# Kernel optimization log

Measured on AMD Instinct MI355X. Metric: run time of the kernel, lower is better.

## Reference

```python
import jax, jax.numpy as jnp
import numpy as np
from jax.ops import segment_sum

NUM_NODES = 100000
HIDDEN = 128
NUM_LAYERS = 3
EDGES = 640000
BN_EPS = 1e-5


def setup_inputs() -> dict:
    key = jax.random.key(0)
    ks = jax.random.split(key, 6)
    edge_index = jax.random.randint(ks[0], (2, EDGES), 0, NUM_NODES, dtype=jnp.int32)
    # xavier-ish init for embedding (hidden-1 dims; last dim is log-degree feature)
    emb_weight = jax.random.normal(ks[1], (NUM_NODES, HIDDEN - 1), dtype=jnp.float32) * 0.02
    # GCNConv linear weights [L, in, out] and biases [L, out]
    Ws = jax.random.normal(ks[2], (NUM_LAYERS, HIDDEN, HIDDEN), dtype=jnp.float32) * (1.0 / np.sqrt(HIDDEN))
    bs = jnp.zeros((NUM_LAYERS, HIDDEN), dtype=jnp.float32)
    gammas = jnp.ones((NUM_LAYERS, HIDDEN), dtype=jnp.float32)
    betas = jnp.zeros((NUM_LAYERS, HIDDEN), dtype=jnp.float32)
    return {"emb_weight": emb_weight, "Ws": Ws, "bs": bs,
            "gammas": gammas, "betas": betas, "edge_index": edge_index}


def reference(emb_weight, Ws, bs, gammas, betas, edge_index):
    row, col = edge_index[0], edge_index[1]  # source, target
    N = emb_weight.shape[0]
    ones_e = jnp.ones(row.shape[0], dtype=emb_weight.dtype)

    # node_degree_features = log(out_degree + 1) (degree of edge_index[0])
    deg_src = segment_sum(ones_e, row, num_segments=N)
    x = jnp.concatenate([emb_weight, jnp.log(deg_src + 1.0)[:, None]], axis=1)  # [N, H]

    # GCN symmetric normalization (add_self_loops=False): deg over targets
    deg = segment_sum(ones_e, col, num_segments=N)
    dinv = jnp.where(deg > 0, jax.lax.rsqrt(jnp.maximum(deg, 1.0)), 0.0)
    norm = dinv[row] * dinv[col]  # [E]

    for i in range(Ws.shape[0]):
        x_prev = x
        h = x @ Ws[i]  # [N, H]
        # scatter-add of normalized messages: out[col] += norm * h[row]
        agg = segment_sum(norm[:, None] * h[row], col, num_segments=N) + bs[i]
        # BatchNorm1d (batch statistics, biased variance)
        mean = agg.mean(axis=0)
        var = agg.var(axis=0)
        x = gammas[i] * (agg - mean) * jax.lax.rsqrt(var + BN_EPS) + betas[i]
        x = jax.nn.relu(x)
        if i > 0:
            x = x + 0.5 * x_prev
    return x
```

## Files before the change

kernel.cpp:

```cpp
#include <hip/hip_runtime.h>
#include <hip/hip_bf16.h>
#include <math.h>

#define BN_EPS 1e-5f

typedef __attribute__((ext_vector_type(8))) short short8v;
typedef __attribute__((ext_vector_type(4))) float f32x4;

__device__ inline float bf_lo(unsigned int p) { return __uint_as_float(p << 16); }
__device__ inline float bf_hi(unsigned int p) { return __uint_as_float(p & 0xffff0000u); }
__device__ inline unsigned int packbf(float a, float b) {
    unsigned short lo = __builtin_bit_cast(unsigned short, __float2bfloat16(a));
    unsigned short hi = __builtin_bit_cast(unsigned short, __float2bfloat16(b));
    return (unsigned int)lo | ((unsigned int)hi << 16);
}


__global__ __launch_bounds__(256) void deg_kernel(const int* __restrict__ row, const int* __restrict__ col,
                                                  float* __restrict__ deg_src, float* __restrict__ deg_dst, int E) {
    int e = blockIdx.x * 256 + threadIdx.x;
    if (e < E) {
        atomicAdd(&deg_src[row[e]], 1.0f);
        atomicAdd(&deg_dst[col[e]], 1.0f);
    }
}

__global__ __launch_bounds__(256) void dinv_cnt_kernel(float* __restrict__ deg_dst, int* __restrict__ cnt, int N) {
    int n = blockIdx.x * 256 + threadIdx.x;
    if (n < N) {
        float d = deg_dst[n];
        cnt[n] = (int)d;
        deg_dst[n] = (d > 0.0f) ? rsqrtf(d) : 0.0f;
    }
}

__global__ __launch_bounds__(256) void initx_kernel(const float* __restrict__ emb, const float* __restrict__ deg_src,
                                                    unsigned int* __restrict__ x, int N) {
    int idx = blockIdx.x * 256 + threadIdx.x;
    if (idx < N * 64) {
        int n = idx >> 6, p = idx & 63;
        float v0, v1;
        if (p < 63) {
            v0 = emb[(size_t)n * 127 + 2 * p];
            v1 = emb[(size_t)n * 127 + 2 * p + 1];
        } else {
            v0 = emb[(size_t)n * 127 + 126];
            v1 = logf(deg_src[n] + 1.0f);
        }
        x[idx] = packbf(v0, v1);
    }
}

__global__ __launch_bounds__(256) void wt_kernel(const float* __restrict__ Ws, __hip_bfloat16* __restrict__ Wt) {
    int idx = blockIdx.x * 256 + threadIdx.x;
    if (idx < 3 * 16384) {
        int l = idx >> 14, rem = idx & 16383, c = rem >> 7, k = rem & 127;
        Wt[idx] = __float2bfloat16(Ws[(l << 14) + (k << 7) + c]);
    }
}


__global__ __launch_bounds__(256) void scan_pass1(const int* __restrict__ cnt, int* __restrict__ blockSums,
                                                  int N, int PT) {
    __shared__ int lds[256];
    const int tid = threadIdx.x;
    const int start = (blockIdx.x * 256 + tid) * PT;
    int s = 0;
    for (int i = 0; i < PT; ++i) {
        int idx = start + i;
        if (idx < N) s += cnt[idx];
    }
    lds[tid] = s;
    __syncthreads();
    for (int d = 128; d > 0; d >>= 1) {
        if (tid < d) lds[tid] += lds[tid + d];
        __syncthreads();
    }
    if (tid == 0) blockSums[blockIdx.x] = lds[0];
}

__global__ __launch_bounds__(256) void scan_pass2(const int* __restrict__ blockSums, int* __restrict__ blockOffs) {
    __shared__ int lds[256];
    const int tid = threadIdx.x;
    int v = blockSums[tid];
    lds[tid] = v;
    __syncthreads();
    for (int d = 1; d < 256; d <<= 1) {
        int t = (tid >= d) ? lds[tid - d] : 0;
        __syncthreads();
        lds[tid] += t;
        __syncthreads();
    }
    blockOffs[tid] = lds[tid] - v;
}

__global__ __launch_bounds__(256) void scan_pass3(const int* __restrict__ cnt, const int* __restrict__ blockOffs,
                                                  int* __restrict__ off, int* __restrict__ cur,
                                                  int N, int PT, int E) {
    __shared__ int lds[256];
    const int tid = threadIdx.x;
    const int start = (blockIdx.x * 256 + tid) * PT;
    int s = 0;
    for (int i = 0; i < PT; ++i) {
        int idx = start + i;
        if (idx < N) s += cnt[idx];
    }
    lds[tid] = s;
    __syncthreads();
    for (int d = 1; d < 256; d <<= 1) {
        int t = (tid >= d) ? lds[tid - d] : 0;
        __syncthreads();
        lds[tid] += t;
        __syncthreads();
    }
    int prefix = blockOffs[blockIdx.x] + lds[tid] - s;
    for (int i = 0; i < PT; ++i) {
        int idx = start + i;
        if (idx < N) {
            off[idx] = prefix;
            cur[idx] = prefix;
            prefix += cnt[idx];
        }
    }
    if (blockIdx.x == 0 && tid == 0) off[N] = E;
}

__global__ __launch_bounds__(256) void fill_kernel(const int* __restrict__ row, const int* __restrict__ col,
                                                   const float* __restrict__ dinv, int* __restrict__ cur,
                                                   int2* __restrict__ meta, int E) {
    int e = blockIdx.x * 256 + threadIdx.x;
    if (e < E) {
        int r = row[e], t = col[e];
        int p = atomicAdd(&cur[t], 1);
        meta[p] = make_int2(r, __float_as_int(dinv[r] * dinv[t]));
    }
}


__global__ __launch_bounds__(256) void gemm_mfma(const __hip_bfloat16* __restrict__ X,
                                                 const __hip_bfloat16* __restrict__ Wt,
                                                 __hip_bfloat16* __restrict__ H, float* __restrict__ sums,
                                                 int nStripes, int N) {
    if (blockIdx.x == 0) sums[threadIdx.x] = 0.0f;

    const int lane = threadIdx.x & 63;
    const int wv = threadIdx.x >> 6;
    const int r = lane & 15;
    const int q = lane >> 4;
    const int ch = (blockIdx.x * 4 + wv) & 1;

    short8v bfrag[4][4];
#pragma unroll
    for (int ct = 0; ct < 4; ++ct)
#pragma unroll
        for (int kk = 0; kk < 4; ++kk)
            bfrag[ct][kk] = *(const short8v*)(Wt + ((ch * 64 + ct * 16 + r) << 7) + kk * 32 + q * 8);

    const int totalJobs = nStripes * 2;
    for (int job = blockIdx.x * 4 + wv; job < totalJobs; job += gridDim.x * 4) {
        const int s = job >> 1;
        const int arow = s * 16 + r;
        short8v a0 = {}, a1 = {}, a2 = {}, a3 = {};
        if (arow < N) {
            const __hip_bfloat16* xp = X + ((size_t)arow << 7) + q * 8;
            a0 = *(const short8v*)(xp);
            a1 = *(const short8v*)(xp + 32);
            a2 = *(const short8v*)(xp + 64);
            a3 = *(const short8v*)(xp + 96);
        }
        f32x4 acc[4];
#pragma unroll
        for (int ct = 0; ct < 4; ++ct) {
            f32x4 c = {0.f, 0.f, 0.f, 0.f};
            c = __builtin_amdgcn_mfma_f32_16x16x32_bf16(a0, bfrag[ct][0], c, 0, 0, 0);
            c = __builtin_amdgcn_mfma_f32_16x16x32_bf16(a1, bfrag[ct][1], c, 0, 0, 0);
            c = __builtin_amdgcn_mfma_f32_16x16x32_bf16(a2, bfrag[ct][2], c, 0, 0, 0);
            c = __builtin_amdgcn_mfma_f32_16x16x32_bf16(a3, bfrag[ct][3], c, 0, 0, 0);
            acc[ct] = c;
        }
#pragma unroll
        for (int g = 0; g < 4; ++g) {
            int grow = s * 16 + q * 4 + g;
            if (grow < N) {
                __hip_bfloat16* hp = H + ((size_t)grow << 7) + ch * 64 + r;
#pragma unroll
                for (int ct = 0; ct < 4; ++ct)
                    hp[ct * 16] = __float2bfloat16(acc[ct][g]);
            }
        }
    }
}


__global__ __launch_bounds__(256) void gather_kernel(const __hip_bfloat16* __restrict__ h,
                                                     const int* __restrict__ off, const int2* __restrict__ meta,
                                                     const float* __restrict__ bias,
                                                     unsigned int* __restrict__ aggb, float* __restrict__ sums, int N) {
    __shared__ float sm[2][4][128];
    const int tid = threadIdx.x;
    const int lane = tid & 63;
    const int w = tid >> 6;
    const int g = lane >> 4;
    const int s = lane & 15;

    float b8[8];
    *(float4*)&b8[0] = *(const float4*)&bias[s * 8];
    *(float4*)&b8[4] = *(const float4*)&bias[s * 8 + 4];

    float psum[8], psq[8];
#pragma unroll
    for (int j = 0; j < 8; ++j) { psum[j] = 0.f; psq[j] = 0.f; }

    for (int base = (blockIdx.x * 4 + w) * 2; base < N; base += gridDim.x * 8) {
        const int nA = __builtin_amdgcn_readfirstlane(base);
        const int hasB = (nA + 1 < N);
        const int sA = off[nA];
        const int eA = off[nA + 1];
        const int eB = hasB ? off[nA + 2] : eA;

        float accA[8], accB[8];
#pragma unroll
        for (int j = 0; j < 8; ++j) { accA[j] = 0.f; accB[j] = 0.f; }

        int iA = sA, iB = eA;
        while (iA < eA || iB < eB) {
            int i0A = iA + g, i1A = iA + 4 + g;
            int i0B = iB + g, i1B = iB + 4 + g;
            int idx0A = (i0A < eA) ? i0A : 0;
            int idx1A = (i1A < eA) ? i1A : 0;
            int idx0B = (i0B < eB) ? i0B : 0;
            int idx1B = (i1B < eB) ? i1B : 0;
            int2 m0A = meta[idx0A], m1A = meta[idx1A];
            int2 m0B = meta[idx0B], m1B = meta[idx1B];
            float w0A = (i0A < eA) ? __int_as_float(m0A.y) : 0.f;
            float w1A = (i1A < eA) ? __int_as_float(m1A.y) : 0.f;
            float w0B = (i0B < eB) ? __int_as_float(m0B.y) : 0.f;
            float w1B = (i1B < eB) ? __int_as_float(m1B.y) : 0.f;
            short8v h0A = *(const short8v*)(h + ((size_t)m0A.x << 7) + s * 8);
            short8v h1A = *(const short8v*)(h + ((size_t)m1A.x << 7) + s * 8);
            short8v h0B = *(const short8v*)(h + ((size_t)m0B.x << 7) + s * 8);
            short8v h1B = *(const short8v*)(h + ((size_t)m1B.x << 7) + s * 8);
#pragma unroll
            for (int j = 0; j < 4; ++j) {
                unsigned int u;
                u = ((const unsigned int*)&h0A)[j];
                accA[2 * j]     = fmaf(w0A, bf_lo(u), accA[2 * j]);
                accA[2 * j + 1] = fmaf(w0A, bf_hi(u), accA[2 * j + 1]);
                u = ((const unsigned int*)&h1A)[j];
                accA[2 * j]     = fmaf(w1A, bf_lo(u), accA[2 * j]);
                accA[2 * j + 1] = fmaf(w1A, bf_hi(u), accA[2 * j + 1]);
                u = ((const unsigned int*)&h0B)[j];
                accB[2 * j]     = fmaf(w0B, bf_lo(u), accB[2 * j]);
                accB[2 * j + 1] = fmaf(w0B, bf_hi(u), accB[2 * j + 1]);
                u = ((const unsigned int*)&h1B)[j];
                accB[2 * j]     = fmaf(w1B, bf_lo(u), accB[2 * j]);
                accB[2 * j + 1] = fmaf(w1B, bf_hi(u), accB[2 * j + 1]);
            }
            iA += 8; iB += 8;
        }
#pragma unroll
        for (int j = 0; j < 8; ++j) {
            accA[j] += __shfl_xor(accA[j], 16);
            accA[j] += __shfl_xor(accA[j], 32);
            accA[j] += b8[j];
            accB[j] += __shfl_xor(accB[j], 16);
            accB[j] += __shfl_xor(accB[j], 32);
            accB[j] += b8[j];
        }
        if (g == 0) {
            unsigned int pk[4];
#pragma unroll
            for (int j = 0; j < 4; ++j) pk[j] = packbf(accA[2 * j], accA[2 * j + 1]);
            *(uint4*)(aggb + ((size_t)nA << 6) + s * 4) = *(uint4*)pk;
#pragma unroll
            for (int j = 0; j < 8; ++j) {
                psum[j] += accA[j];
                psq[j] = fmaf(accA[j], accA[j], psq[j]);
            }
            if (hasB) {
#pragma unroll
                for (int j = 0; j < 8; ++j) {
                    psum[j] += accB[j];
                    psq[j] = fmaf(accB[j], accB[j], psq[j]);
                }
            }
        } else if (g == 1 && hasB) {
            unsigned int pk[4];
#pragma unroll
            for (int j = 0; j < 4; ++j) pk[j] = packbf(accB[2 * j], accB[2 * j + 1]);
            *(uint4*)(aggb + ((size_t)(nA + 1) << 6) + s * 4) = *(uint4*)pk;
        }
    }
    if (g == 0) {
#pragma unroll
        for (int j = 0; j < 8; ++j) {
            sm[0][w][s * 8 + j] = psum[j];
            sm[1][w][s * 8 + j] = psq[j];
        }
    }
    __syncthreads();
    if (tid < 128) {
        atomicAdd(&sums[tid], sm[0][0][tid] + sm[0][1][tid] + sm[0][2][tid] + sm[0][3][tid]);
    } else {
        int c = tid - 128;
        atomicAdd(&sums[128 + c], sm[1][0][c] + sm[1][1][c] + sm[1][2][c] + sm[1][3][c]);
    }
}


template <int MODE>
__global__ __launch_bounds__(256) void bn_apply(const uint4* __restrict__ aggb, const float* __restrict__ sums,
                                                const float* __restrict__ gamma, const float* __restrict__ beta,
                                                const uint4* __restrict__ xprev, void* __restrict__ xout,
                                                int NO, float invN) {
    int idx = blockIdx.x * 256 + threadIdx.x;
    if (idx >= NO) return;
    const int c0 = (idx & 15) * 8;

    float su[8], sq[8], gm[8], bt[8];
    *(float4*)&su[0] = *(const float4*)&sums[c0];
    *(float4*)&su[4] = *(const float4*)&sums[c0 + 4];
    *(float4*)&sq[0] = *(const float4*)&sums[128 + c0];
    *(float4*)&sq[4] = *(const float4*)&sums[128 + c0 + 4];
    *(float4*)&gm[0] = *(const float4*)&gamma[c0];
    *(float4*)&gm[4] = *(const float4*)&gamma[c0 + 4];
    *(float4*)&bt[0] = *(const float4*)&beta[c0];
    *(float4*)&bt[4] = *(const float4*)&beta[c0 + 4];

    float sc[8], sh[8];
#pragma unroll
    for (int j = 0; j < 8; ++j) {
        float m = su[j] * invN;
        float v = sq[j] * invN - m * m;
        float inv = rsqrtf(fmaxf(v, 0.0f) + BN_EPS);
        sc[j] = gm[j] * inv;
        sh[j] = bt[j] - m * sc[j];
    }

    uint4 av = aggb[idx];
    const unsigned int* au = (const unsigned int*)&av;
    float r[8];
#pragma unroll
    for (int j = 0; j < 4; ++j) {
        r[2 * j]     = fmaxf(fmaf(bf_lo(au[j]), sc[2 * j],     sh[2 * j]),     0.f);
        r[2 * j + 1] = fmaxf(fmaf(bf_hi(au[j]), sc[2 * j + 1], sh[2 * j + 1]), 0.f);
    }
    if (MODE >= 1) {
        uint4 xv = xprev[idx];
        const unsigned int* xu = (const unsigned int*)&xv;
#pragma unroll
        for (int j = 0; j < 4; ++j) {
            r[2 * j]     = fmaf(0.5f, bf_lo(xu[j]), r[2 * j]);
            r[2 * j + 1] = fmaf(0.5f, bf_hi(xu[j]), r[2 * j + 1]);
        }
    }
    if (MODE == 2) {
        float* op = (float*)xout + (size_t)idx * 8;
        *(float4*)op       = make_float4(r[0], r[1], r[2], r[3]);
        *(float4*)(op + 4) = make_float4(r[4], r[5], r[6], r[7]);
    } else {
        unsigned int pk[4];
#pragma unroll
        for (int j = 0; j < 4; ++j) pk[j] = packbf(r[2 * j], r[2 * j + 1]);
        ((uint4*)xout)[idx] = *(uint4*)pk;
    }
}


extern "C" void kernel_launch(void* const* d_in, const int* in_sizes, int n_in,
                              void* d_out, int out_size, void* d_ws, size_t ws_size,
                              hipStream_t stream) {
    const float* emb    = (const float*)d_in[0];
    const float* Ws     = (const float*)d_in[1];
    const float* bs     = (const float*)d_in[2];
    const float* gammas = (const float*)d_in[3];
    const float* betas  = (const float*)d_in[4];
    const int*   ei     = (const int*)d_in[5];

    const int N = in_sizes[0] / 127;
    const int E = in_sizes[5] / 2;
    const int* row = ei;
    const int* col = ei + E;
    float* out = (float*)d_out;

    const size_t NH = (size_t)N * 128;
    __hip_bfloat16* XA = (__hip_bfloat16*)d_ws;
    __hip_bfloat16* XB = XA + NH;
    unsigned int*  AGG = (unsigned int*)(XB + NH);
    int2*         meta = (int2*)(AGG + NH / 2);
    __hip_bfloat16* Wt = (__hip_bfloat16*)(meta + E);
    float* deg_src = (float*)(Wt + 3 * 16384);
    float* dinvb   = deg_src + N;
    float* sums    = dinvb + N;
    int*   cnt     = (int*)(sums + 256);
    int*   cur     = cnt + N;
    int*   blockSums = cur + N;
    int*   blockOffs = blockSums + 256;
    int*   off     = blockOffs + 256;

    const int NO = (int)(NH / 8);
    const int PT = (N + 65535) / 65536;
    const int nStripes = (N + 15) / 16;
    const float invN = 1.0f / (float)N;

    hipMemsetAsync(deg_src, 0, sizeof(float) * 2 * (size_t)N, stream);
    wt_kernel<<<(3 * 16384 + 255) / 256, 256, 0, stream>>>(Ws, Wt);
    deg_kernel<<<(E + 255) / 256, 256, 0, stream>>>(row, col, deg_src, dinvb, E);
    dinv_cnt_kernel<<<(N + 255) / 256, 256, 0, stream>>>(dinvb, cnt, N);
    initx_kernel<<<(N * 64 + 255) / 256, 256, 0, stream>>>(emb, deg_src, (unsigned int*)XA, N);
    scan_pass1<<<256, 256, 0, stream>>>(cnt, blockSums, N, PT);
    scan_pass2<<<1, 256, 0, stream>>>(blockSums, blockOffs);
    scan_pass3<<<256, 256, 0, stream>>>(cnt, blockOffs, off, cur, N, PT, E);
    fill_kernel<<<(E + 255) / 256, 256, 0, stream>>>(row, col, dinvb, cur, meta, E);

    const __hip_bfloat16* xin[3]  = {XA, XA, XB};
    __hip_bfloat16*       hbuf[3] = {XB, XB, XA};

    for (int i = 0; i < 3; ++i) {
        gemm_mfma<<<1024, 256, 0, stream>>>(xin[i], Wt + (size_t)i * 16384, hbuf[i], sums, nStripes, N);
        gather_kernel<<<2048, 256, 0, stream>>>(hbuf[i], off, meta, bs + i * 128, AGG, sums, N);
        if (i == 0)
            bn_apply<0><<<(NO + 255) / 256, 256, 0, stream>>>((const uint4*)AGG, sums, gammas, betas,
                                                              (const uint4*)xin[i], (void*)XA, NO, invN);
        else if (i == 1)
            bn_apply<1><<<(NO + 255) / 256, 256, 0, stream>>>((const uint4*)AGG, sums, gammas + 128, betas + 128,
                                                              (const uint4*)xin[i], (void*)XB, NO, invN);
        else
            bn_apply<2><<<(NO + 255) / 256, 256, 0, stream>>>((const uint4*)AGG, sums, gammas + 256, betas + 256,
                                                              (const uint4*)xin[i], (void*)out, NO, invN);
    }
}
```

Before: 445.7 us.

## Map one node per 16-lane group in gather and fold dinv into fill

The gather kernel now gives each 16-lane quarter-wave its own destination node (4 nodes per wave), instead of splitting each node's edges across the four lane groups and combining them with shuffles. Each group issues up to 8 independent meta and row loads up front for more memory-level parallelism, then runs a serial tail loop for higher-degree nodes. The separate dinv/count kernel is dropped: the scan reads float degrees directly and fill computes the rsqrt inline. The workspace is also reordered so the int4 offset loads are aligned. The per-node serial tail adds divergence inside a wave when node degrees differ.

```diff
diff --git a/kernel.cpp b/kernel.cpp
--- a/kernel.cpp
+++ b/kernel.cpp
@@ -22,15 +22,6 @@
     if (e < E) {
         atomicAdd(&deg_src[row[e]], 1.0f);
         atomicAdd(&deg_dst[col[e]], 1.0f);
-    }
-}
-
-__global__ __launch_bounds__(256) void dinv_cnt_kernel(float* __restrict__ deg_dst, int* __restrict__ cnt, int N) {
-    int n = blockIdx.x * 256 + threadIdx.x;
-    if (n < N) {
-        float d = deg_dst[n];
-        cnt[n] = (int)d;
-        deg_dst[n] = (d > 0.0f) ? rsqrtf(d) : 0.0f;
     }
 }
 
@@ -60,7 +51,7 @@
 }
 
 
-__global__ __launch_bounds__(256) void scan_pass1(const int* __restrict__ cnt, int* __restrict__ blockSums,
+__global__ __launch_bounds__(256) void scan_pass1(const float* __restrict__ deg, int* __restrict__ blockSums,
                                                   int N, int PT) {
     __shared__ int lds[256];
     const int tid = threadIdx.x;
@@ -68,7 +59,7 @@
     int s = 0;
     for (int i = 0; i < PT; ++i) {
         int idx = start + i;
-        if (idx < N) s += cnt[idx];
+        if (idx < N) s += (int)deg[idx];
     }
     lds[tid] = s;
     __syncthreads();
@@ -94,7 +85,7 @@
     blockOffs[tid] = lds[tid] - v;
 }
 
-__global__ __launch_bounds__(256) void scan_pass3(const int* __restrict__ cnt, const int* __restrict__ blockOffs,
+__global__ __launch_bounds__(256) void scan_pass3(const float* __restrict__ deg, const int* __restrict__ blockOffs,
                                                   int* __restrict__ off, int* __restrict__ cur,
                                                   int N, int PT, int E) {
     __shared__ int lds[256];
@@ -103,7 +94,7 @@
     int s = 0;
     for (int i = 0; i < PT; ++i) {
         int idx = start + i;
-        if (idx < N) s += cnt[idx];
+        if (idx < N) s += (int)deg[idx];
     }
     lds[tid] = s;
     __syncthreads();
@@ -119,20 +110,23 @@
         if (idx < N) {
             off[idx] = prefix;
             cur[idx] = prefix;
-            prefix += cnt[idx];
+            prefix += (int)deg[idx];
         }
     }
     if (blockIdx.x == 0 && tid == 0) off[N] = E;
 }
 
 __global__ __launch_bounds__(256) void fill_kernel(const int* __restrict__ row, const int* __restrict__ col,
-                                                   const float* __restrict__ dinv, int* __restrict__ cur,
+                                                   const float* __restrict__ deg_dst, int* __restrict__ cur,
                                                    int2* __restrict__ meta, int E) {
     int e = blockIdx.x * 256 + threadIdx.x;
     if (e < E) {
         int r = row[e], t = col[e];
         int p = atomicAdd(&cur[t], 1);
-        meta[p] = make_int2(r, __float_as_int(dinv[r] * dinv[t]));
+        float dr = deg_dst[r], dt = deg_dst[t];
+        float ir = (dr > 0.0f) ? rsqrtf(dr) : 0.0f;
+        float it = (dt > 0.0f) ? rsqrtf(dt) : 0.0f;
+        meta[p] = make_int2(r, __float_as_int(ir * it));
     }
 }
 
@@ -211,85 +205,75 @@
 #pragma unroll
     for (int j = 0; j < 8; ++j) { psum[j] = 0.f; psq[j] = 0.f; }
 
-    for (int base = (blockIdx.x * 4 + w) * 2; base < N; base += gridDim.x * 8) {
+    for (int base = (blockIdx.x * 4 + w) * 4; base < N; base += gridDim.x * 16) {
         const int nA = __builtin_amdgcn_readfirstlane(base);
-        const int hasB = (nA + 1 < N);
-        const int sA = off[nA];
-        const int eA = off[nA + 1];
-        const int eB = hasB ? off[nA + 2] : eA;
-
-        float accA[8], accB[8];
-#pragma unroll
-        for (int j = 0; j < 8; ++j) { accA[j] = 0.f; accB[j] = 0.f; }
-
-        int iA = sA, iB = eA;
-        while (iA < eA || iB < eB) {
-            int i0A = iA + g, i1A = iA + 4 + g;
-            int i0B = iB + g, i1B = iB + 4 + g;
-            int idx0A = (i0A < eA) ? i0A : 0;
-            int idx1A = (i1A < eA) ? i1A : 0;
-            int idx0B = (i0B < eB) ? i0B : 0;
-            int idx1B = (i1B < eB) ? i1B : 0;
-            int2 m0A = meta[idx0A], m1A = meta[idx1A];
-            int2 m0B = meta[idx0B], m1B = meta[idx1B];
-            float w0A = (i0A < eA) ? __int_as_float(m0A.y) : 0.f;
-            float w1A = (i1A < eA) ? __int_as_float(m1A.y) : 0.f;
-            float w0B = (i0B < eB) ? __int_as_float(m0B.y) : 0.f;
-            float w1B = (i1B < eB) ? __int_as_float(m1B.y) : 0.f;
-            short8v h0A = *(const short8v*)(h + ((size_t)m0A.x << 7) + s * 8);
-            short8v h1A = *(const short8v*)(h + ((size_t)m1A.x << 7) + s * 8);
-            short8v h0B = *(const short8v*)(h + ((size_t)m0B.x << 7) + s * 8);
-            short8v h1B = *(const short8v*)(h + ((size_t)m1B.x << 7) + s * 8);
+        int4 o4 = *(const int4*)&off[nA];
+        int  o5 = off[nA + 4];
+        const bool nodeValid = (nA + g) < N;
+        int sG = (g < 2) ? ((g == 0) ? o4.x : o4.y) : ((g == 2) ? o4.z : o4.w);
+        int eG = (g < 2) ? ((g == 0) ? o4.y : o4.z) : ((g == 2) ? o4.w : o5);
+        if (!nodeValid) { sG = 0; eG = 0; }
+
+        int   rr[8];
+        float wgt[8];
+#pragma unroll
+        for (int t = 0; t < 8; ++t) {
+            int i = sG + t;
+            int idx = (i < eG) ? i : 0;
+            int2 m = meta[idx];
+            rr[t] = m.x;
+            wgt[t] = (i < eG) ? __int_as_float(m.y) : 0.0f;
+        }
+        uint4 hv[8];
+#pragma unroll
+        for (int t = 0; t < 8; ++t)
+            hv[t] = *(const uint4*)(h + ((size_t)rr[t] << 7) + s * 8);
+
+        float acc[8];
+#pragma unroll
+        for (int j = 0; j < 8; ++j) acc[j] = 0.f;
+#pragma unroll
+        for (int t = 0; t < 8; ++t) {
+            const unsigned int* u = (const unsigned int*)&hv[t];
 #pragma unroll
             for (int j = 0; j < 4; ++j) {
-                unsigned int u;
-                u = ((const unsigned int*)&h0A)[j];
-                accA[2 * j]     = fmaf(w0A, bf_lo(u), accA[2 * j]);
-                accA[2 * j + 1] = fmaf(w0A, bf_hi(u), accA[2 * j + 1]);
-                u = ((const unsigned int*)&h1A)[j];
-                accA[2 * j]     = fmaf(w1A, bf_lo(u), accA[2 * j]);
-                accA[2 * j + 1] = fmaf(w1A, bf_hi(u), accA[2 * j + 1]);
-                u = ((const unsigned int*)&h0B)[j];
-                accB[2 * j]     = fmaf(w0B, bf_lo(u), accB[2 * j]);
-                accB[2 * j + 1] = fmaf(w0B, bf_hi(u), accB[2 * j + 1]);
-                u = ((const unsigned int*)&h1B)[j];
-                accB[2 * j]     = fmaf(w1B, bf_lo(u), accB[2 * j]);
-                accB[2 * j + 1] = fmaf(w1B, bf_hi(u), accB[2 * j + 1]);
+                acc[2 * j]     = fmaf(wgt[t], bf_lo(u[j]), acc[2 * j]);
+                acc[2 * j + 1] = fmaf(wgt[t], bf_hi(u[j]), acc[2 * j + 1]);
             }
-            iA += 8; iB += 8;
-        }
-#pragma unroll
-        for (int j = 0; j < 8; ++j) {
-            accA[j] += __shfl_xor(accA[j], 16);
-            accA[j] += __shfl_xor(accA[j], 32);
-            accA[j] += b8[j];
-            accB[j] += __shfl_xor(accB[j], 16);
-            accB[j] += __shfl_xor(accB[j], 32);
-            accB[j] += b8[j];
-        }
-        if (g == 0) {
+        }
+        for (int i = sG + 8; i < eG; ++i) {
+            int2 m = meta[i];
+            float wv = __int_as_float(m.y);
+            uint4 hh = *(const uint4*)(h + ((size_t)m.x << 7) + s * 8);
+            const unsigned int* u = (const unsigned int*)&hh;
+#pragma unroll
+            for (int j = 0; j < 4; ++j) {
+                acc[2 * j]     = fmaf(wv, bf_lo(u[j]), acc[2 * j]);
+                acc[2 * j + 1] = fmaf(wv, bf_hi(u[j]), acc[2 * j + 1]);
+            }
+        }
+#pragma unroll
+        for (int j = 0; j < 8; ++j) acc[j] += b8[j];
+
+        if (nodeValid) {
             unsigned int pk[4];
 #pragma unroll
-            for (int j = 0; j < 4; ++j) pk[j] = packbf(accA[2 * j], accA[2 * j + 1]);
-            *(uint4*)(aggb + ((size_t)nA << 6) + s * 4) = *(uint4*)pk;
+            for (int j = 0; j < 4; ++j) pk[j] = packbf(acc[2 * j], acc[2 * j + 1]);
+            *(uint4*)(aggb + ((size_t)(nA + g) << 6) + s * 4) = *(uint4*)pk;
 #pragma unroll
             for (int j = 0; j < 8; ++j) {
-                psum[j] += accA[j];
-                psq[j] = fmaf(accA[j], accA[j], psq[j]);
+                psum[j] += acc[j];
+                psq[j] = fmaf(acc[j], acc[j], psq[j]);
             }
-            if (hasB) {
-#pragma unroll
-                for (int j = 0; j < 8; ++j) {
-                    psum[j] += accB[j];
-                    psq[j] = fmaf(accB[j], accB[j], psq[j]);
-                }
-            }
-        } else if (g == 1 && hasB) {
-            unsigned int pk[4];
-#pragma unroll
-            for (int j = 0; j < 4; ++j) pk[j] = packbf(accB[2 * j], accB[2 * j + 1]);
-            *(uint4*)(aggb + ((size_t)(nA + 1) << 6) + s * 4) = *(uint4*)pk;
-        }
+        }
+    }
+
+#pragma unroll
+    for (int j = 0; j < 8; ++j) {
+        psum[j] += __shfl_xor(psum[j], 16);
+        psum[j] += __shfl_xor(psum[j], 32);
+        psq[j]  += __shfl_xor(psq[j], 16);
+        psq[j]  += __shfl_xor(psq[j], 32);
     }
     if (g == 0) {
 #pragma unroll
@@ -387,16 +371,18 @@
     __hip_bfloat16* XA = (__hip_bfloat16*)d_ws;
     __hip_bfloat16* XB = XA + NH;
     unsigned int*  AGG = (unsigned int*)(XB + NH);
-    int2*         meta = (int2*)(AGG + NH / 2);
-    __hip_bfloat16* Wt = (__hip_bfloat16*)(meta + E);
-    float* deg_src = (float*)(Wt + 3 * 16384);
-    float* dinvb   = deg_src + N;
-    float* sums    = dinvb + N;
-    int*   cnt     = (int*)(sums + 256);
-    int*   cur     = cnt + N;
-    int*   blockSums = cur + N;
+    int*   off      = (int*)(AGG + NH / 2);
+    const int offPad = (N + 8) & ~3;
+    int*   cur      = off + offPad;
+    const int curPad = (N + 4) & ~3;
+    int*   blockSums = cur + curPad;
     int*   blockOffs = blockSums + 256;
-    int*   off     = blockOffs + 256;
+    float* sums     = (float*)(blockOffs + 256);
+    int2*  meta     = (int2*)(sums + 256);
+    const int Ep = (E + 1) & ~1;
+    __hip_bfloat16* Wt = (__hip_bfloat16*)(meta + Ep);
+    float* deg_src  = (float*)(Wt + 3 * 16384);
+    float* deg_dst  = deg_src + N;
 
     const int NO = (int)(NH / 8);
     const int PT = (N + 65535) / 65536;
@@ -405,13 +391,12 @@
 
     hipMemsetAsync(deg_src, 0, sizeof(float) * 2 * (size_t)N, stream);
     wt_kernel<<<(3 * 16384 + 255) / 256, 256, 0, stream>>>(Ws, Wt);
-    deg_kernel<<<(E + 255) / 256, 256, 0, stream>>>(row, col, deg_src, dinvb, E);
-    dinv_cnt_kernel<<<(N + 255) / 256, 256, 0, stream>>>(dinvb, cnt, N);
+    deg_kernel<<<(E + 255) / 256, 256, 0, stream>>>(row, col, deg_src, deg_dst, E);
     initx_kernel<<<(N * 64 + 255) / 256, 256, 0, stream>>>(emb, deg_src, (unsigned int*)XA, N);
-    scan_pass1<<<256, 256, 0, stream>>>(cnt, blockSums, N, PT);
+    scan_pass1<<<256, 256, 0, stream>>>(deg_dst, blockSums, N, PT);
     scan_pass2<<<1, 256, 0, stream>>>(blockSums, blockOffs);
-    scan_pass3<<<256, 256, 0, stream>>>(cnt, blockOffs, off, cur, N, PT, E);
-    fill_kernel<<<(E + 255) / 256, 256, 0, stream>>>(row, col, dinvb, cur, meta, E);
+    scan_pass3<<<256, 256, 0, stream>>>(deg_dst, blockOffs, off, cur, N, PT, E);
+    fill_kernel<<<(E + 255) / 256, 256, 0, stream>>>(row, col, deg_dst, cur, meta, E);
 
     const __hip_bfloat16* xin[3]  = {XA, XA, XB};
     __hip_bfloat16*       hbuf[3] = {XB, XB, XA};
```

Result: slower. 551.0 us (+23.6%).

## Prefetch next GEMM A-tiles and CSR offsets, fold dinv kernel into consumers

Applied to the files above, without the earlier changes.

Removes the separate dinv/count kernel: the scan passes read the float degree directly and fill_kernel computes rsqrt normalization inline. The MFMA GEMM now software-pipelines loads of the next stripe's A fragments while computing the current one. The gather kernel prefetches the next iteration's CSR offsets as int2 loads, which needs aligned, padded off arrays, so the workspace layout is reordered. This saves one launch and hides some load latency, at the cost of extra registers and redundant rsqrt work per edge.

```diff
diff --git a/kernel.cpp b/kernel.cpp
--- a/kernel.cpp
+++ b/kernel.cpp
@@ -22,15 +22,6 @@
     if (e < E) {
         atomicAdd(&deg_src[row[e]], 1.0f);
         atomicAdd(&deg_dst[col[e]], 1.0f);
-    }
-}
-
-__global__ __launch_bounds__(256) void dinv_cnt_kernel(float* __restrict__ deg_dst, int* __restrict__ cnt, int N) {
-    int n = blockIdx.x * 256 + threadIdx.x;
-    if (n < N) {
-        float d = deg_dst[n];
-        cnt[n] = (int)d;
-        deg_dst[n] = (d > 0.0f) ? rsqrtf(d) : 0.0f;
     }
 }
 
@@ -60,7 +51,7 @@
 }
 
 
-__global__ __launch_bounds__(256) void scan_pass1(const int* __restrict__ cnt, int* __restrict__ blockSums,
+__global__ __launch_bounds__(256) void scan_pass1(const float* __restrict__ deg, int* __restrict__ blockSums,
                                                   int N, int PT) {
     __shared__ int lds[256];
     const int tid = threadIdx.x;
@@ -68,7 +59,7 @@
     int s = 0;
     for (int i = 0; i < PT; ++i) {
         int idx = start + i;
-        if (idx < N) s += cnt[idx];
+        if (idx < N) s += (int)deg[idx];
     }
     lds[tid] = s;
     __syncthreads();
@@ -94,7 +85,7 @@
     blockOffs[tid] = lds[tid] - v;
 }
 
-__global__ __launch_bounds__(256) void scan_pass3(const int* __restrict__ cnt, const int* __restrict__ blockOffs,
+__global__ __launch_bounds__(256) void scan_pass3(const float* __restrict__ deg, const int* __restrict__ blockOffs,
                                                   int* __restrict__ off, int* __restrict__ cur,
                                                   int N, int PT, int E) {
     __shared__ int lds[256];
@@ -103,7 +94,7 @@
     int s = 0;
     for (int i = 0; i < PT; ++i) {
         int idx = start + i;
-        if (idx < N) s += cnt[idx];
+        if (idx < N) s += (int)deg[idx];
     }
     lds[tid] = s;
     __syncthreads();
@@ -119,20 +110,25 @@
         if (idx < N) {
             off[idx] = prefix;
             cur[idx] = prefix;
-            prefix += cnt[idx];
-        }
-    }
-    if (blockIdx.x == 0 && tid == 0) off[N] = E;
+            prefix += (int)deg[idx];
+        }
+    }
+    if (blockIdx.x == 0 && tid == 0) {
+        off[N] = E; off[N + 1] = E; off[N + 2] = E; off[N + 3] = E;
+    }
 }
 
 __global__ __launch_bounds__(256) void fill_kernel(const int* __restrict__ row, const int* __restrict__ col,
-                                                   const float* __restrict__ dinv, int* __restrict__ cur,
+                                                   const float* __restrict__ deg_dst, int* __restrict__ cur,
                                                    int2* __restrict__ meta, int E) {
     int e = blockIdx.x * 256 + threadIdx.x;
     if (e < E) {
         int r = row[e], t = col[e];
         int p = atomicAdd(&cur[t], 1);
-        meta[p] = make_int2(r, __float_as_int(dinv[r] * dinv[t]));
+        float dr = deg_dst[r], dt = deg_dst[t];
+        float ir = (dr > 0.0f) ? rsqrtf(dr) : 0.0f;
+        float it = (dt > 0.0f) ? rsqrtf(dt) : 0.0f;
+        meta[p] = make_int2(r, __float_as_int(ir * it));
     }
 }
 
@@ -157,10 +153,13 @@
             bfrag[ct][kk] = *(const short8v*)(Wt + ((ch * 64 + ct * 16 + r) << 7) + kk * 32 + q * 8);
 
     const int totalJobs = nStripes * 2;
-    for (int job = blockIdx.x * 4 + wv; job < totalJobs; job += gridDim.x * 4) {
-        const int s = job >> 1;
-        const int arow = s * 16 + r;
-        short8v a0 = {}, a1 = {}, a2 = {}, a3 = {};
+    const int jstep = gridDim.x * 4;
+    int job = blockIdx.x * 4 + wv;
+    if (job >= totalJobs) return;
+
+    short8v a0 = {}, a1 = {}, a2 = {}, a3 = {};
+    {
+        const int arow = (job >> 1) * 16 + r;
         if (arow < N) {
             const __hip_bfloat16* xp = X + ((size_t)arow << 7) + q * 8;
             a0 = *(const short8v*)(xp);
@@ -168,6 +167,23 @@
             a2 = *(const short8v*)(xp + 64);
             a3 = *(const short8v*)(xp + 96);
         }
+    }
+    while (true) {
+        const int jn = job + jstep;
+        const bool hasNext = jn < totalJobs;
+        short8v n0 = {}, n1 = {}, n2 = {}, n3 = {};
+        {
+            const int pj = hasNext ? jn : job;
+            const int arow = (pj >> 1) * 16 + r;
+            if (arow < N) {
+                const __hip_bfloat16* xp = X + ((size_t)arow << 7) + q * 8;
+                n0 = *(const short8v*)(xp);
+                n1 = *(const short8v*)(xp + 32);
+                n2 = *(const short8v*)(xp + 64);
+                n3 = *(const short8v*)(xp + 96);
+            }
+        }
+        const int s = job >> 1;
         f32x4 acc[4];
 #pragma unroll
         for (int ct = 0; ct < 4; ++ct) {
@@ -188,6 +204,9 @@
                     hp[ct * 16] = __float2bfloat16(acc[ct][g]);
             }
         }
+        if (!hasNext) break;
+        a0 = n0; a1 = n1; a2 = n2; a3 = n3;
+        job = jn;
     }
 }
 
@@ -211,12 +230,25 @@
 #pragma unroll
     for (int j = 0; j < 8; ++j) { psum[j] = 0.f; psq[j] = 0.f; }
 
-    for (int base = (blockIdx.x * 4 + w) * 2; base < N; base += gridDim.x * 8) {
+    const int b0 = (blockIdx.x * 4 + w) * 2;
+    const int bstep = gridDim.x * 8;
+    int2 curA = make_int2(0, 0), curB = make_int2(0, 0);
+    if (b0 < N) {
+        curA = *(const int2*)&off[b0];
+        curB = *(const int2*)&off[b0 + 2];
+    }
+
+    for (int base = b0; base < N; base += bstep) {
         const int nA = __builtin_amdgcn_readfirstlane(base);
+        const int nxt = base + bstep;
+        const int pn = (nxt < N) ? nxt : 0;
+        int2 nxtA = *(const int2*)&off[pn];
+        int2 nxtB = *(const int2*)&off[pn + 2];
+
         const int hasB = (nA + 1 < N);
-        const int sA = off[nA];
-        const int eA = off[nA + 1];
-        const int eB = hasB ? off[nA + 2] : eA;
+        const int sA = curA.x;
+        const int eA = curA.y;
+        const int eB = hasB ? curB.x : eA;
 
         float accA[8], accB[8];
 #pragma unroll
@@ -290,6 +322,7 @@
             for (int j = 0; j < 4; ++j) pk[j] = packbf(accB[2 * j], accB[2 * j + 1]);
             *(uint4*)(aggb + ((size_t)(nA + 1) << 6) + s * 4) = *(uint4*)pk;
         }
+        curA = nxtA; curB = nxtB;
     }
     if (g == 0) {
 #pragma unroll
@@ -387,16 +420,18 @@
     __hip_bfloat16* XA = (__hip_bfloat16*)d_ws;
     __hip_bfloat16* XB = XA + NH;
     unsigned int*  AGG = (unsigned int*)(XB + NH);
-    int2*         meta = (int2*)(AGG + NH / 2);
-    __hip_bfloat16* Wt = (__hip_bfloat16*)(meta + E);
-    float* deg_src = (float*)(Wt + 3 * 16384);
-    float* dinvb   = deg_src + N;
-    float* sums    = dinvb + N;
-    int*   cnt     = (int*)(sums + 256);
-    int*   cur     = cnt + N;
-    int*   blockSums = cur + N;
+    int*   off      = (int*)(AGG + NH / 2);
+    const int offPad = (N + 8) & ~3;
+    int*   cur      = off + offPad;
+    const int curPad = (N + 4) & ~3;
+    int*   blockSums = cur + curPad;
     int*   blockOffs = blockSums + 256;
-    int*   off     = blockOffs + 256;
+    float* sums     = (float*)(blockOffs + 256);
+    int2*  meta     = (int2*)(sums + 256);
+    const int Ep = (E + 1) & ~1;
+    __hip_bfloat16* Wt = (__hip_bfloat16*)(meta + Ep);
+    float* deg_src  = (float*)(Wt + 3 * 16384);
+    float* deg_dst  = deg_src + N;
 
     const int NO = (int)(NH / 8);
     const int PT = (N + 65535) / 65536;
@@ -405,13 +440,12 @@
 
     hipMemsetAsync(deg_src, 0, sizeof(float) * 2 * (size_t)N, stream);
     wt_kernel<<<(3 * 16384 + 255) / 256, 256, 0, stream>>>(Ws, Wt);
-    deg_kernel<<<(E + 255) / 256, 256, 0, stream>>>(row, col, deg_src, dinvb, E);
-    dinv_cnt_kernel<<<(N + 255) / 256, 256, 0, stream>>>(dinvb, cnt, N);
+    deg_kernel<<<(E + 255) / 256, 256, 0, stream>>>(row, col, deg_src, deg_dst, E);
     initx_kernel<<<(N * 64 + 255) / 256, 256, 0, stream>>>(emb, deg_src, (unsigned int*)XA, N);
-    scan_pass1<<<256, 256, 0, stream>>>(cnt, blockSums, N, PT);
+    scan_pass1<<<256, 256, 0, stream>>>(deg_dst, blockSums, N, PT);
     scan_pass2<<<1, 256, 0, stream>>>(blockSums, blockOffs);
-    scan_pass3<<<256, 256, 0, stream>>>(cnt, blockOffs, off, cur, N, PT, E);
-    fill_kernel<<<(E + 255) / 256, 256, 0, stream>>>(row, col, dinvb, cur, meta, E);
+    scan_pass3<<<256, 256, 0, stream>>>(deg_dst, blockOffs, off, cur, N, PT, E);
+    fill_kernel<<<(E + 255) / 256, 256, 0, stream>>>(row, col, deg_dst, cur, meta, E);
 
     const __hip_bfloat16* xin[3]  = {XA, XA, XB};
     __hip_bfloat16*       hbuf[3] = {XB, XB, XA};
```

Result: slower. 572.1 us (+28.3%).
